# Performance work log

Measured on AMD Instinct MI355X. Metric: run time of the kernel, lower is better.

The kernel has to match this reference:

```python
import jax, jax.numpy as jnp
import numpy as np

HIDDEN = 2048
HEADS = 16
HEAD_DIM = HIDDEN // HEADS
ROPE_BASE = 10000.0


def rope_cos_sin(seq_len, dim, dtype=jnp.float32):
    inv_freq = 1.0 / (ROPE_BASE ** (jnp.arange(0, dim, 2, dtype=jnp.float32) / dim))
    t = jnp.arange(seq_len, dtype=jnp.float32)
    freqs = jnp.einsum('i,j->ij', t, inv_freq)            # [S, dim/2]
    emb = jnp.concatenate([freqs, freqs], axis=-1)        # [S, dim]
    return jnp.cos(emb).astype(dtype), jnp.sin(emb).astype(dtype)


def rotate_half(x):
    x1, x2 = jnp.split(x, 2, axis=-1)
    return jnp.concatenate([-x2, x1], axis=-1)


def setup_inputs() -> dict:
    key = jax.random.key(0)
    ks = jax.random.split(key, 6)
    B, S, D = 2, 2048, HIDDEN
    scale = 1.0 / np.sqrt(D)
    x = jax.random.normal(ks[0], (B, S, D), dtype=jnp.float32)
    Wq = jax.random.normal(ks[1], (D, D), dtype=jnp.float32) * scale
    Wk = jax.random.normal(ks[2], (D, D), dtype=jnp.float32) * scale
    Wv = jax.random.normal(ks[3], (D, D), dtype=jnp.float32) * scale
    Wo = jax.random.normal(ks[4], (D, D), dtype=jnp.float32) * scale
    bo = jnp.zeros((D,), dtype=jnp.float32)
    return {"x": x, "Wq": Wq, "Wk": Wk, "Wv": Wv, "Wo": Wo, "bo": bo}


def reference(x, Wq, Wk, Wv, Wo, bo):
    B, S, D = x.shape
    H, Dh = HEADS, HEAD_DIM
    # torch Linear: x @ W.T
    q = (x @ Wq.T).reshape(B, S, H, Dh).transpose(0, 2, 1, 3)  # [B,H,S,Dh]
    k = (x @ Wk.T).reshape(B, S, H, Dh).transpose(0, 2, 1, 3)
    v = (x @ Wv.T).reshape(B, S, H, Dh).transpose(0, 2, 1, 3)
    cos, sin = rope_cos_sin(S, Dh, x.dtype)                    # [S, Dh]
    q = q * cos + rotate_half(q) * sin
    k = k * cos + rotate_half(k) * sin
    scale = Dh ** -0.5
    attn = jnp.einsum('bhqd,bhkd->bhqk', q, k) * scale
    attn = jax.nn.softmax(attn, axis=-1)
    out = jnp.einsum('bhqk,bhkd->bhqd', attn, v)               # [B,H,S,Dh]
    out = out.transpose(0, 2, 1, 3).reshape(B, S, D)
    return out @ Wo.T + bo
```

## Files before the change

kernel.cpp:

```cpp
#include <hip/hip_runtime.h>
#include <stdint.h>


#define SEQ 2048
#define HD 128
#define DMODEL 2048

typedef __bf16 bf16x8 __attribute__((ext_vector_type(8)));
typedef float f32x4 __attribute__((ext_vector_type(4)));
typedef unsigned short u16;
typedef unsigned int u32;

typedef bf16x8 __attribute__((may_alias)) bf16x8_a;
typedef uint2 __attribute__((may_alias)) uint2_a;

__device__ __forceinline__ u16 f2bf(float f) {
  unsigned int u = __float_as_uint(f);
  u += 0x7fff + ((u >> 16) & 1);
  return (u16)(u >> 16);
}
__device__ __forceinline__ float bf2f(u16 v) {
  return __uint_as_float(((unsigned int)v) << 16);
}

typedef __attribute__((address_space(1))) void* gas_t;
typedef __attribute__((address_space(3))) void* las_t;
__device__ __forceinline__ void load_lds16(const void* g, void* l) {
  __builtin_amdgcn_global_load_lds((gas_t)(uintptr_t)g,
                                   (las_t)(uint32_t)(uintptr_t)l, 16, 0, 0);
}

__global__ void conv_all(const float* __restrict__ x,
                         const float* __restrict__ wq,
                         const float* __restrict__ wk,
                         const float* __restrict__ wv,
                         const float* __restrict__ wo,
                         u16* __restrict__ xb, u16* __restrict__ wqkv,
                         u16* __restrict__ wob) {
  int i = blockIdx.x * 256 + threadIdx.x;
  const float* src;
  u16* dst;
  int off;
  if (i < 2097152) { src = x; dst = xb; off = i; }
  else if (i < 3145728) { src = wq; dst = wqkv; off = i - 2097152; }
  else if (i < 4194304) { src = wk; dst = wqkv + 4194304; off = i - 3145728; }
  else if (i < 5242880) { src = wv; dst = wqkv + 8388608; off = i - 4194304; }
  else { src = wo; dst = wob; off = i - 5242880; }
  float4 v = ((const float4*)src)[off];
  ushort4 o;
  o.x = f2bf(v.x); o.y = f2bf(v.y); o.z = f2bf(v.z); o.w = f2bf(v.w);
  ((ushort4*)dst)[off] = o;
}

template <int MODE>
__global__ __launch_bounds__(256, 3)
void gemm_nt(const u16* __restrict__ A, const u16* __restrict__ Bm,
             void* __restrict__ Cout, const float* __restrict__ bias,
             int N, int K) {
  __shared__ __align__(16) u16 Asl[128 * 64];
  __shared__ __align__(16) u16 Bsl[128 * 64];
  const int tid = threadIdx.x;
  const int lane = tid & 63;
  const int wave = tid >> 6;
  const int quad = lane >> 4;
  const int l15 = lane & 15;
  const int row0 = blockIdx.y * 128;
  const int col0 = blockIdx.x * 128;
  const int waveM = (wave & 1) * 64;
  const int waveN = (wave >> 1) * 64;

  f32x4 acc[4][4] = {};

  for (int k0 = 0; k0 < K; k0 += 64) {
    __syncthreads();
#pragma unroll
    for (int j = 0; j < 4; ++j) {
      int idx = (wave * 4 + j) * 64 + lane;
      int r = idx >> 3;
      int c8 = (idx & 7) ^ (r & 7);
      load_lds16(A + (size_t)(row0 + r) * K + (k0 + c8 * 8), &Asl[idx * 8]);
      load_lds16(Bm + (size_t)(col0 + r) * K + (k0 + c8 * 8), &Bsl[idx * 8]);
    }
    __syncthreads();
#pragma unroll
    for (int c = 0; c < 2; ++c) {
      bf16x8 af[4], bfr[4];
#pragma unroll
      for (int mt = 0; mt < 4; ++mt) {
        int r = waveM + mt * 16 + l15;
        af[mt] = *(const bf16x8*)&Asl[(r * 8 + ((c * 4 + quad) ^ (r & 7))) * 8];
      }
#pragma unroll
      for (int nt = 0; nt < 4; ++nt) {
        int r = waveN + nt * 16 + l15;
        bfr[nt] = *(const bf16x8*)&Bsl[(r * 8 + ((c * 4 + quad) ^ (r & 7))) * 8];
      }
#pragma unroll
      for (int mt = 0; mt < 4; ++mt)
#pragma unroll
        for (int nt = 0; nt < 4; ++nt)
          acc[mt][nt] = __builtin_amdgcn_mfma_f32_16x16x32_bf16(
              af[mt], bfr[nt], acc[mt][nt], 0, 0, 0);
    }
  }

  if (MODE == 0) {
    u16* Cq = (u16*)Cout;
    const int which = col0 >> 11;
    const int h = (col0 >> 7) & 15;
#pragma unroll
    for (int mt = 0; mt < 4; ++mt) {
#pragma unroll
      for (int nt = 0; nt < 4; ++nt) {
        int d = waveN + nt * 16 + l15;
#pragma unroll
        for (int r = 0; r < 4; ++r) {
          int row = row0 + waveM + mt * 16 + quad * 4 + r;
          int b = row >> 11, s = row & 2047;
          size_t off = ((((size_t)which * 2 + b) * 16 + h) * SEQ + s) * HD + d;
          Cq[off] = f2bf(acc[mt][nt][r]);
        }
      }
    }
  } else {
    float* C = (float*)Cout;
#pragma unroll
    for (int nt = 0; nt < 4; ++nt) {
      int d = col0 + waveN + nt * 16 + l15;
      float bv = bias[d];
#pragma unroll
      for (int mt = 0; mt < 4; ++mt) {
#pragma unroll
        for (int r = 0; r < 4; ++r) {
          int row = row0 + waveM + mt * 16 + quad * 4 + r;
          C[(size_t)row * N + d] = acc[mt][nt][r] + bv;
        }
      }
    }
  }
}

__global__ void rope_kernel(u16* __restrict__ qkv) {
  int idx = blockIdx.x * 256 + threadIdx.x;
  int j = idx & 63;
  int row = idx >> 6;
  int s = row & 2047;
  u16* p = qkv + (size_t)row * HD;
  float x1 = bf2f(p[j]);
  float x2 = bf2f(p[j + 64]);
  float inv = exp2f(-0.2076205059304601f * (float)j);
  float th = (float)s * inv;
  float sn, cs;
  sincosf(th, &sn, &cs);
  float qs = (row < 65536) ? 0.12751744f : 1.0f;
  p[j] = f2bf((x1 * cs - x2 * sn) * qs);
  p[j + 64] = f2bf((x2 * cs + x1 * sn) * qs);
}

__global__ void transpose_v(const u16* __restrict__ vraw, u16* __restrict__ vt) {
  __shared__ u16 t[64][65];
  int s0 = blockIdx.x * 64;
  int d0 = blockIdx.y * 64;
  int bh = blockIdx.z;
  const u16* src = vraw + (size_t)bh * SEQ * HD;
  u16* dst = vt + (size_t)bh * HD * SEQ;
#pragma unroll
  for (int i = 0; i < 16; ++i) {
    int idx = i * 256 + threadIdx.x;
    int r = idx >> 6, c = idx & 63;
    t[r][c] = src[(size_t)(s0 + r) * HD + d0 + c];
  }
  __syncthreads();
#pragma unroll
  for (int i = 0; i < 16; ++i) {
    int idx = i * 256 + threadIdx.x;
    int r = idx >> 6, c = idx & 63;
    dst[(size_t)(d0 + r) * SEQ + s0 + c] = t[c][r];
  }
}

__global__ __launch_bounds__(256, 2)
void attn_kernel(const u16* __restrict__ qkv, const u16* __restrict__ vt,
                 u16* __restrict__ attn_out) {
  __shared__ __align__(16) u16 Kl[64 * 128];
  __shared__ __align__(16) u16 Vl[128 * 64];
  __shared__ __align__(16) u16 Ol[16 * 64];
  __shared__ __align__(16) u16 Pl[4][32 * 64];

  const int tid = threadIdx.x;
  const int lane = tid & 63;
  const int wave = tid >> 6;
  const int quad = lane >> 4;
  const int l15 = lane & 15;
  const int q0 = blockIdx.x * 128;
  const int bh = blockIdx.y;
  const size_t SD = (size_t)SEQ * HD;

  {
    u16 val = (tid < 16) ? (u16)0x3F80 : (u16)0;
    ushort4 ov; ov.x = val; ov.y = val; ov.z = val; ov.w = val;
    *(ushort4*)&Ol[tid * 4] = ov;
  }

  const u16* Q = qkv + (size_t)bh * SD;
  const u16* Kg = qkv + (size_t)(32 + bh) * SD;
  const u16* Vg = vt + (size_t)bh * SD;

  bf16x8 qf[2][4];
#pragma unroll
  for (int mt = 0; mt < 2; ++mt) {
    int qrow = q0 + wave * 32 + mt * 16 + l15;
#pragma unroll
    for (int c = 0; c < 4; ++c)
      qf[mt][c] = *(const bf16x8*)(Q + (size_t)qrow * HD + c * 32 + quad * 8);
  }

  f32x4 of[9][2] = {};
  float m_i[2] = {-3.0e38f, -3.0e38f};
  u16* pw = &Pl[wave][0];

  for (int kv0 = 0; kv0 < SEQ; kv0 += 64) {
    __syncthreads();
#pragma unroll
    for (int j = 0; j < 4; ++j) {
      int idx = (wave * 4 + j) * 64 + lane;
      {
        int r = idx >> 4, cs = idx & 15;
        int cc = cs ^ (r & 15);
        load_lds16(Kg + (size_t)(kv0 + r) * HD + cc * 8, &Kl[idx * 8]);
      }
      {
        int r = idx >> 3, cs = idx & 7;
        int cc = cs ^ (r & 7);
        load_lds16(Vg + (size_t)r * SEQ + kv0 + cc * 8, &Vl[idx * 8]);
      }
    }
    __syncthreads();

    f32x4 sc[4][2] = {};
#pragma unroll
    for (int c = 0; c < 4; ++c) {
      bf16x8 kf[4];
#pragma unroll
      for (int nt = 0; nt < 4; ++nt)
        kf[nt] = *(const bf16x8*)&Kl[((nt * 16 + l15) * 16 +
                                      ((c * 4 + quad) ^ l15)) * 8];
#pragma unroll
      for (int nt = 0; nt < 4; ++nt)
#pragma unroll
        for (int mt = 0; mt < 2; ++mt)
          sc[nt][mt] = __builtin_amdgcn_mfma_f32_16x16x32_bf16(
              kf[nt], qf[mt][c], sc[nt][mt], 0, 0, 0);
    }

    float alpha[2];
#pragma unroll
    for (int mt = 0; mt < 2; ++mt) {
      float mx = sc[0][mt][0];
#pragma unroll
      for (int nt = 0; nt < 4; ++nt)
#pragma unroll
        for (int r = 0; r < 4; ++r) mx = fmaxf(mx, sc[nt][mt][r]);
      mx = fmaxf(mx, __shfl_xor(mx, 16));
      mx = fmaxf(mx, __shfl_xor(mx, 32));
      float mn = fmaxf(m_i[mt], mx);
      alpha[mt] = exp2f(m_i[mt] - mn);
      m_i[mt] = mn;
    }

#pragma unroll
    for (int nt = 0; nt < 4; ++nt) {
#pragma unroll
      for (int mt = 0; mt < 2; ++mt) {
        float p0 = exp2f(sc[nt][mt][0] - m_i[mt]);
        float p1 = exp2f(sc[nt][mt][1] - m_i[mt]);
        float p2 = exp2f(sc[nt][mt][2] - m_i[mt]);
        float p3 = exp2f(sc[nt][mt][3] - m_i[mt]);
        u32 lo = __builtin_amdgcn_perm(__float_as_uint(p1),
                                       __float_as_uint(p0), 0x07060302u);
        u32 hi = __builtin_amdgcn_perm(__float_as_uint(p3),
                                       __float_as_uint(p2), 0x07060302u);
        int row = mt * 16 + l15;
        int a = nt * 2 + (quad >> 1);
        int idx16 = (row * 8 + (a ^ (l15 & 7))) * 8 + (quad & 1) * 4;
        uint2 pk; pk.x = lo; pk.y = hi;
        *(uint2_a*)&pw[idx16] = pk;
      }
    }

#pragma unroll
    for (int dt = 0; dt < 9; ++dt)
#pragma unroll
      for (int mt = 0; mt < 2; ++mt) of[dt][mt] = of[dt][mt] * alpha[mt];

#pragma unroll
    for (int c = 0; c < 2; ++c) {
      bf16x8 pf[2];
#pragma unroll
      for (int mt = 0; mt < 2; ++mt)
        pf[mt] = *(const bf16x8_a*)&pw[((mt * 16 + l15) * 8 +
                                        ((c * 4 + quad) ^ (l15 & 7))) * 8];
#pragma unroll
      for (int dt = 0; dt < 9; ++dt) {
        bf16x8 vf =
            (dt < 8)
                ? *(const bf16x8*)&Vl[((dt * 16 + l15) * 8 +
                                       ((c * 4 + quad) ^ (l15 & 7))) * 8]
                : *(const bf16x8*)&Ol[(l15 * 8 +
                                       ((c * 4 + quad) ^ (l15 & 7))) * 8];
#pragma unroll
        for (int mt = 0; mt < 2; ++mt)
          of[dt][mt] = __builtin_amdgcn_mfma_f32_16x16x32_bf16(
              vf, pf[mt], of[dt][mt], 0, 0, 0);
      }
    }
  }

  const int b = bh >> 4, h = bh & 15;
#pragma unroll
  for (int mt = 0; mt < 2; ++mt) {
    float lsum = __shfl(of[8][mt][0], l15, 64);
    float inv = 1.f / lsum;
    int s = q0 + wave * 32 + mt * 16 + l15;
    size_t rowb = ((size_t)b * SEQ + s) * DMODEL + h * HD;
#pragma unroll
    for (int dt = 0; dt < 8; ++dt) {
      ushort4 ov;
      ov.x = f2bf(of[dt][mt][0] * inv);
      ov.y = f2bf(of[dt][mt][1] * inv);
      ov.z = f2bf(of[dt][mt][2] * inv);
      ov.w = f2bf(of[dt][mt][3] * inv);
      *(ushort4*)&attn_out[rowb + dt * 16 + quad * 4] = ov;
    }
  }
}

extern "C" void kernel_launch(void* const* d_in, const int* in_sizes, int n_in,
                              void* d_out, int out_size, void* d_ws,
                              size_t ws_size, hipStream_t stream) {
  const float* x = (const float*)d_in[0];
  const float* Wq = (const float*)d_in[1];
  const float* Wk = (const float*)d_in[2];
  const float* Wv = (const float*)d_in[3];
  const float* Wo = (const float*)d_in[4];
  const float* bo = (const float*)d_in[5];
  float* out = (float*)d_out;

  char* ws = (char*)d_ws;
  u16* xb = (u16*)(ws);
  u16* wqkv = (u16*)(ws + (size_t)(16 << 20));
  u16* wob = (u16*)(ws + (size_t)(40 << 20));
  u16* qkv = (u16*)(ws + (size_t)(48 << 20));
  u16* vt = wqkv;
  u16* attn = xb;

  conv_all<<<24576, 256, 0, stream>>>(x, Wq, Wk, Wv, Wo, xb, wqkv, wob);

  gemm_nt<0><<<dim3(48, 32), 256, 0, stream>>>(xb, wqkv, qkv, nullptr, 6144,
                                               2048);
  rope_kernel<<<32768, 256, 0, stream>>>(qkv);
  transpose_v<<<dim3(32, 2, 32), 256, 0, stream>>>(qkv + (size_t)64 * SEQ * HD,
                                                   vt);
  attn_kernel<<<dim3(16, 32), 256, 0, stream>>>(qkv, vt, attn);
  gemm_nt<1><<<dim3(16, 32), 256, 0, stream>>>(attn, wob, out, bo, 2048, 2048);
}
```

Before: 405.5 us.

## Fuse RoPE and V transpose into QKV GEMM epilogue via LDS staging

The QKV projection is split into two launches. The Q/K launch applies RoPE and the query scale in its epilogue, staging the tile through swizzled LDS and writing 16-byte vectors with hardware sin/cos. The V launch swaps the MFMA operands so it writes V already transposed, which removes the separate rope and transpose kernels and their extra global round trips. The attention kernel also builds its ones-vector for the row-sum in registers instead of reading it from LDS. In exchange the epilogue gains an LDS pass and two barriers, and the hardware sin/cos with a fractional revolution argument may be less accurate than sincosf.

After: 379.4 us. 6.4% less time.

```diff
diff --git a/kernel.cpp b/kernel.cpp
--- a/kernel.cpp
+++ b/kernel.cpp
@@ -13,6 +13,7 @@
 
 typedef bf16x8 __attribute__((may_alias)) bf16x8_a;
 typedef uint2 __attribute__((may_alias)) uint2_a;
+typedef uint4 __attribute__((may_alias)) uint4_a;
 
 __device__ __forceinline__ u16 f2bf(float f) {
   unsigned int u = __float_as_uint(f);
@@ -56,16 +57,17 @@
 __global__ __launch_bounds__(256, 3)
 void gemm_nt(const u16* __restrict__ A, const u16* __restrict__ Bm,
              void* __restrict__ Cout, const float* __restrict__ bias,
-             int N, int K) {
-  __shared__ __align__(16) u16 Asl[128 * 64];
-  __shared__ __align__(16) u16 Bsl[128 * 64];
+             int colbase, int N, int K) {
+  __shared__ __align__(16) u16 Smem[2][128 * 64];
+  u16* Asl = Smem[0];
+  u16* Bsl = Smem[1];
   const int tid = threadIdx.x;
   const int lane = tid & 63;
   const int wave = tid >> 6;
   const int quad = lane >> 4;
   const int l15 = lane & 15;
   const int row0 = blockIdx.y * 128;
-  const int col0 = blockIdx.x * 128;
+  const int col0 = colbase + blockIdx.x * 128;
   const int waveM = (wave & 1) * 64;
   const int waveN = (wave >> 1) * 64;
 
@@ -98,31 +100,18 @@
 #pragma unroll
       for (int mt = 0; mt < 4; ++mt)
 #pragma unroll
-        for (int nt = 0; nt < 4; ++nt)
-          acc[mt][nt] = __builtin_amdgcn_mfma_f32_16x16x32_bf16(
-              af[mt], bfr[nt], acc[mt][nt], 0, 0, 0);
-    }
-  }
-
-  if (MODE == 0) {
-    u16* Cq = (u16*)Cout;
-    const int which = col0 >> 11;
-    const int h = (col0 >> 7) & 15;
-#pragma unroll
-    for (int mt = 0; mt < 4; ++mt) {
-#pragma unroll
-      for (int nt = 0; nt < 4; ++nt) {
-        int d = waveN + nt * 16 + l15;
-#pragma unroll
-        for (int r = 0; r < 4; ++r) {
-          int row = row0 + waveM + mt * 16 + quad * 4 + r;
-          int b = row >> 11, s = row & 2047;
-          size_t off = ((((size_t)which * 2 + b) * 16 + h) * SEQ + s) * HD + d;
-          Cq[off] = f2bf(acc[mt][nt][r]);
+        for (int nt = 0; nt < 4; ++nt) {
+          if (MODE == 2)
+            acc[mt][nt] = __builtin_amdgcn_mfma_f32_16x16x32_bf16(
+                bfr[nt], af[mt], acc[mt][nt], 0, 0, 0);
+          else
+            acc[mt][nt] = __builtin_amdgcn_mfma_f32_16x16x32_bf16(
+                af[mt], bfr[nt], acc[mt][nt], 0, 0, 0);
         }
-      }
-    }
-  } else {
+    }
+  }
+
+  if (MODE == 1) {
     float* C = (float*)Cout;
 #pragma unroll
     for (int nt = 0; nt < 4; ++nt) {
@@ -137,45 +126,81 @@
         }
       }
     }
-  }
-}
-
-__global__ void rope_kernel(u16* __restrict__ qkv) {
-  int idx = blockIdx.x * 256 + threadIdx.x;
-  int j = idx & 63;
-  int row = idx >> 6;
-  int s = row & 2047;
-  u16* p = qkv + (size_t)row * HD;
-  float x1 = bf2f(p[j]);
-  float x2 = bf2f(p[j + 64]);
-  float inv = exp2f(-0.2076205059304601f * (float)j);
-  float th = (float)s * inv;
-  float sn, cs;
-  sincosf(th, &sn, &cs);
-  float qs = (row < 65536) ? 0.12751744f : 1.0f;
-  p[j] = f2bf((x1 * cs - x2 * sn) * qs);
-  p[j + 64] = f2bf((x2 * cs + x1 * sn) * qs);
-}
-
-__global__ void transpose_v(const u16* __restrict__ vraw, u16* __restrict__ vt) {
-  __shared__ u16 t[64][65];
-  int s0 = blockIdx.x * 64;
-  int d0 = blockIdx.y * 64;
-  int bh = blockIdx.z;
-  const u16* src = vraw + (size_t)bh * SEQ * HD;
-  u16* dst = vt + (size_t)bh * HD * SEQ;
-#pragma unroll
-  for (int i = 0; i < 16; ++i) {
-    int idx = i * 256 + threadIdx.x;
-    int r = idx >> 6, c = idx & 63;
-    t[r][c] = src[(size_t)(s0 + r) * HD + d0 + c];
-  }
+    return;
+  }
+
+  u16* Cq = (u16*)Cout;
+  const int which = col0 >> 11;
+  const int h = (col0 >> 7) & 15;
+  const int brow = row0 >> 11;
+  const int sbase = row0 & 2047;
+  const float qs = (MODE == 0 && which == 0) ? 0.12751744f : 1.0f;
+
   __syncthreads();
-#pragma unroll
-  for (int i = 0; i < 16; ++i) {
-    int idx = i * 256 + threadIdx.x;
-    int r = idx >> 6, c = idx & 63;
-    dst[(size_t)(d0 + r) * SEQ + s0 + c] = t[c][r];
+  u16* tile = &Smem[0][0];
+#pragma unroll
+  for (int mt = 0; mt < 4; ++mt) {
+#pragma unroll
+    for (int nt = 0; nt < 4; ++nt) {
+#pragma unroll
+      for (int r = 0; r < 4; ++r) {
+        int dd, ss, el;
+        if (MODE == 2) {
+          dd = waveN + nt * 16 + quad * 4 + r;
+          ss = waveM + mt * 16 + l15;
+          el = dd * 128 + (((ss >> 3) ^ (dd & 15)) * 8) + (ss & 7);
+        } else {
+          dd = waveN + nt * 16 + l15;
+          ss = waveM + mt * 16 + quad * 4 + r;
+          el = ss * 128 + (((dd >> 3) ^ (ss & 15)) * 8) + (dd & 7);
+        }
+        tile[el] = f2bf(acc[mt][nt][r] * qs);
+      }
+    }
+  }
+  __syncthreads();
+
+  const int a = lane & 7;
+  const int sg = lane >> 3;
+  if (MODE == 0) {
+    const float c1 = 0.2076205059304601f;
+    const float c2 = 2.6514961294723187f;
+#pragma unroll
+    for (int pass = 0; pass < 4; ++pass) {
+      int s_l = pass * 32 + wave * 8 + sg;
+      int sw = s_l & 15;
+      bf16x8 x1 = *(const bf16x8_a*)&tile[s_l * 128 + ((a ^ sw) * 8)];
+      bf16x8 x2 = *(const bf16x8_a*)&tile[s_l * 128 + (((a + 8) ^ sw) * 8)];
+      int s2048 = sbase + s_l;
+      u16 o1[8], o2[8];
+#pragma unroll
+      for (int e = 0; e < 8; ++e) {
+        float j = (float)(a * 8 + e);
+        float rev = (float)s2048 * __builtin_amdgcn_exp2f(-c1 * j - c2);
+        rev = __builtin_amdgcn_fractf(rev);
+        float sn = __builtin_amdgcn_sinf(rev);
+        float cs = __builtin_amdgcn_cosf(rev);
+        float v1 = (float)x1[e], v2 = (float)x2[e];
+        o1[e] = f2bf(v1 * cs - v2 * sn);
+        o2[e] = f2bf(v2 * cs + v1 * sn);
+      }
+      size_t base =
+          ((((size_t)which * 2 + brow) * 16 + h) * SEQ + s2048) * HD + a * 8;
+      *(uint4_a*)&Cq[base] = *(uint4*)o1;
+      *(uint4_a*)&Cq[base + 64] = *(uint4*)o2;
+    }
+  } else {
+#pragma unroll
+    for (int pass = 0; pass < 4; ++pass) {
+      int d_l = pass * 32 + wave * 8 + sg;
+      int dw = d_l & 15;
+      bf16x8 y1 = *(const bf16x8_a*)&tile[d_l * 128 + ((a ^ dw) * 8)];
+      bf16x8 y2 = *(const bf16x8_a*)&tile[d_l * 128 + (((a + 8) ^ dw) * 8)];
+      size_t base =
+          (((size_t)brow * 16 + h) * HD + d_l) * SEQ + sbase + a * 8;
+      *(uint4_a*)&Cq[base] = *(uint4_a*)&y1;
+      *(uint4_a*)&Cq[base + 64] = *(uint4_a*)&y2;
+    }
   }
 }
 
@@ -184,7 +209,6 @@
                  u16* __restrict__ attn_out) {
   __shared__ __align__(16) u16 Kl[64 * 128];
   __shared__ __align__(16) u16 Vl[128 * 64];
-  __shared__ __align__(16) u16 Ol[16 * 64];
   __shared__ __align__(16) u16 Pl[4][32 * 64];
 
   const int tid = threadIdx.x;
@@ -196,15 +220,13 @@
   const int bh = blockIdx.y;
   const size_t SD = (size_t)SEQ * HD;
 
-  {
-    u16 val = (tid < 16) ? (u16)0x3F80 : (u16)0;
-    ushort4 ov; ov.x = val; ov.y = val; ov.z = val; ov.w = val;
-    *(ushort4*)&Ol[tid * 4] = ov;
-  }
-
   const u16* Q = qkv + (size_t)bh * SD;
   const u16* Kg = qkv + (size_t)(32 + bh) * SD;
   const u16* Vg = vt + (size_t)bh * SD;
+
+  bf16x8 onesf;
+#pragma unroll
+  for (int e = 0; e < 8; ++e) onesf[e] = (l15 == 0) ? (__bf16)1.0f : (__bf16)0.0f;
 
   bf16x8 qf[2][4];
 #pragma unroll
@@ -302,12 +324,10 @@
                                         ((c * 4 + quad) ^ (l15 & 7))) * 8];
 #pragma unroll
       for (int dt = 0; dt < 9; ++dt) {
-        bf16x8 vf =
-            (dt < 8)
-                ? *(const bf16x8*)&Vl[((dt * 16 + l15) * 8 +
-                                       ((c * 4 + quad) ^ (l15 & 7))) * 8]
-                : *(const bf16x8*)&Ol[(l15 * 8 +
-                                       ((c * 4 + quad) ^ (l15 & 7))) * 8];
+        bf16x8 vf = (dt < 8)
+                        ? *(const bf16x8*)&Vl[((dt * 16 + l15) * 8 +
+                                               ((c * 4 + quad) ^ (l15 & 7))) * 8]
+                        : onesf;
 #pragma unroll
         for (int mt = 0; mt < 2; ++mt)
           of[dt][mt] = __builtin_amdgcn_mfma_f32_16x16x32_bf16(
@@ -351,16 +371,16 @@
   u16* wqkv = (u16*)(ws + (size_t)(16 << 20));
   u16* wob = (u16*)(ws + (size_t)(40 << 20));
   u16* qkv = (u16*)(ws + (size_t)(48 << 20));
-  u16* vt = wqkv;
+  u16* vt = qkv + (size_t)2 * 8388608;
   u16* attn = xb;
 
   conv_all<<<24576, 256, 0, stream>>>(x, Wq, Wk, Wv, Wo, xb, wqkv, wob);
 
-  gemm_nt<0><<<dim3(48, 32), 256, 0, stream>>>(xb, wqkv, qkv, nullptr, 6144,
+  gemm_nt<0><<<dim3(32, 32), 256, 0, stream>>>(xb, wqkv, qkv, nullptr, 0,
+                                               6144, 2048);
+  gemm_nt<2><<<dim3(16, 32), 256, 0, stream>>>(xb, wqkv, vt, nullptr, 4096,
+                                               6144, 2048);
+  attn_kernel<<<dim3(16, 32), 256, 0, stream>>>(qkv, vt, attn);
+  gemm_nt<1><<<dim3(16, 32), 256, 0, stream>>>(attn, wob, out, bo, 0, 2048,
                                                2048);
-  rope_kernel<<<32768, 256, 0, stream>>>(qkv);
-  transpose_v<<<dim3(32, 2, 32), 256, 0, stream>>>(qkv + (size_t)64 * SEQ * HD,
-                                                   vt);
-  attn_kernel<<<dim3(16, 32), 256, 0, stream>>>(qkv, vt, attn);
-  gemm_nt<1><<<dim3(16, 32), 256, 0, stream>>>(attn, wob, out, bo, 2048, 2048);
-}
+}
```
